# Kernel tuning notes

Hardware: AMD Instinct MI355X
Metric: run time of the kernel (lower is better)

Reference implementation:

```python
import jax, jax.numpy as jnp
import numpy as np

NX, NY, NZ = 432, 496, 1
D = 64        # num_pt_features
K = 3         # NUM_K
M = 1024      # memory size
BEV = 128     # num_bev_features
NCOORD = 3
NV = 10000    # pillars in scene
NP = 16384    # points in scene
BN_EPS = 1e-3
SHRINK = 0.0025


def hard_shrink_relu(x, lambd, eps=1e-12):
    return jax.nn.relu(x - lambd) * x / (jnp.abs(x - lambd) + eps)


def batchnorm_train(x, gamma, beta, eps=BN_EPS):
    # torch BatchNorm1d training-mode math (biased variance)
    mu = jnp.mean(x, axis=0)
    var = jnp.mean((x - mu) ** 2, axis=0)
    return (x - mu) * jax.lax.rsqrt(var + eps) * gamma + beta


def pdist2(a, b, eps=1e-5):
    # sqrt(eps + |  ||a||^2 + ||b||^2 - 2 a.b |), shape [n1, n2]
    n1 = jnp.sum(a * a, axis=1, keepdims=True)
    n2 = jnp.sum(b * b, axis=1, keepdims=True)
    d2 = n1 + n2.T - 2.0 * (a @ b.T)
    return jnp.sqrt(eps + jnp.abs(d2))


def memory_lookup(x_flat, mem_w, shrink):
    # MemAE-style memory unit: softmax addressing + hard shrink + L1 renorm
    att = jax.nn.softmax(x_flat @ mem_w.T, axis=1)          # [N, M]
    att = hard_shrink_relu(att, shrink)
    att = att / jnp.maximum(jnp.sum(jnp.abs(att), axis=1, keepdims=True), 1e-12)
    return att @ mem_w                                       # [N, D]


def setup_inputs() -> dict:
    key = jax.random.key(0)
    ks = jax.random.split(key, 8)
    rng = np.random.default_rng(0)
    flat = rng.choice(NX * NY, size=NV, replace=False)       # unique BEV cells
    x = (flat % NX).astype(np.int32)
    y = (flat // NX).astype(np.int32)
    coords = jnp.asarray(np.stack([np.zeros(NV, np.int32), x, y,
                                   np.zeros(NV, np.int32)], axis=1))  # (b, x, y, z)
    pc = jax.random.uniform(ks[1], (NP, 4), dtype=jnp.float32)
    point_coords = pc * jnp.array([0.0, NX, NY, 1.0], dtype=jnp.float32)
    return {
        "pillar_features": jax.random.normal(ks[0], (NV, D), dtype=jnp.float32),
        "coords": coords,
        "point_features": jax.random.normal(ks[2], (NP, D), dtype=jnp.float32),
        "point_coords": point_coords,
        "adapt_w": jax.random.normal(ks[3], (BEV // 2, D * K), dtype=jnp.float32) * 0.05,
        "bn1_g": jnp.ones((BEV // 2,), dtype=jnp.float32),
        "bn1_b": jnp.zeros((BEV // 2,), dtype=jnp.float32),
        "weight_w": jax.random.normal(ks[4], (2, BEV // 2), dtype=jnp.float32) * 0.1,
        "bn2_g": jnp.ones((2,), dtype=jnp.float32),
        "bn2_b": jnp.zeros((2,), dtype=jnp.float32),
        "mem_w": jax.random.normal(ks[5], (M, D), dtype=jnp.float32) * 0.1,
    }


def reference(pillar_features, coords, point_features, point_coords,
              adapt_w, bn1_g, bn1_b, weight_w, bn2_g, bn2_b, mem_w):
    nv = pillar_features.shape[0]
    pillars = pillar_features.T                              # [D, nv]

    # --- coord-based retrieval: smallest-K pdist(pillar coords, point coords) ---
    dist = pdist2(coords.astype(jnp.float32), point_coords)  # [nv, np]
    _, idx_c = jax.lax.top_k(-dist, K)                       # [nv, K]
    pillars_positive_coord = point_features[idx_c]           # [nv, K, D]

    # --- feature-based retrieval: top-K of softmax(points @ pillars, axis=0) ---
    score = jax.nn.softmax(point_features @ pillars, axis=0) # [np, nv]
    _, idx_f = jax.lax.top_k(score.T, K)                     # [nv, K]
    points_positive = point_features[idx_f]                  # [nv, K, D]

    # --- memory unit on both branches ---
    out_f = memory_lookup(points_positive.reshape(nv * K, D), mem_w, SHRINK).reshape(nv, K * D)
    out_c = memory_lookup(pillars_positive_coord.reshape(nv * K, D), mem_w, SHRINK).reshape(nv, K * D)

    f = jax.nn.relu(batchnorm_train(out_f @ adapt_w.T, bn1_g, bn1_b))  # [nv, 64]
    c = jax.nn.relu(batchnorm_train(out_c @ adapt_w.T, bn1_g, bn1_b))  # [nv, 64]
    w = jax.nn.softmax(batchnorm_train(pillar_features @ weight_w.T, bn2_g, bn2_b), axis=-1)
    pillars_aug = w[:, :1] * f + w[:, 1:2] * c               # [nv, 64]
    pillars_full = jnp.concatenate([pillars, pillars_aug.T], axis=0)  # [128, nv]

    # --- scatter to BEV canvas ---
    bev_idx = coords[:, 1] + coords[:, 2] * NX + coords[:, 3]
    spatial = jnp.zeros((BEV, NX * NY), dtype=pillar_features.dtype).at[:, bev_idx].set(pillars_full)
    pind = jnp.zeros((NCOORD, NX * NY), dtype=pillar_features.dtype)
    pind = pind.at[0, bev_idx].set(coords[:, 2].astype(jnp.float32))
    pind = pind.at[1, bev_idx].set(coords[:, 3].astype(jnp.float32))
    pind = pind.at[2, bev_idx].set(coords[:, 1].astype(jnp.float32))

    spatial_features = spatial.reshape(1, BEV * NZ, NY, NX)
    spatial_indices = pind.reshape(1, NCOORD * NZ, NY, NX)
    return spatial_features, spatial_indices
```

## Files before the change

### kernel.cpp

```cpp
#include <hip/hip_runtime.h>
#include <math.h>

#define NXc 432
#define NYc 496
#define NVc 10000
#define NPc 16384
#define CELLS (NXc*NYc)
#define SHRINKc 0.0025f
#define NVPAD 10048
#define NBX 27
#define NBY 31
#define NBIN (NBX*NBY)

typedef unsigned short u16;
typedef __attribute__((ext_vector_type(8))) short s16x8;
typedef __attribute__((ext_vector_type(4))) float f32x4;

__device__ __forceinline__ unsigned med3u(unsigned a, unsigned b, unsigned c) {
    unsigned d;
    asm("v_med3_u32 %0, %1, %2, %3" : "=v"(d) : "v"(a), "v"(b), "v"(c));
    return d;
}

__device__ __forceinline__ u16 f2b(float x) {
    unsigned u = __float_as_uint(x);
    unsigned r = (u + 0x7fffu + ((u >> 16) & 1u)) >> 16;
    return (u16)r;
}

__global__ __launch_bounds__(256) void k_init(const float* __restrict__ pillar,
                                              const float* __restrict__ pfeat,
                                              const float* __restrict__ memw,
                                              const float* __restrict__ adapt,
                                              float* __restrict__ stats,
                                              int* __restrict__ cellMap,
                                              u16* __restrict__ pillarH,
                                              u16* __restrict__ pfeatH,
                                              u16* __restrict__ memwH,
                                              u16* __restrict__ memwTH,
                                              u16* __restrict__ badaptH) {
    int gid = blockIdx.x * 256 + threadIdx.x;
    if (gid < CELLS) cellMap[gid] = -1;
    if (gid < 260) stats[gid] = 0.f;
    const int N1 = NVPAD * 64;
    const int N2 = N1 + NPc * 64;
    const int N3 = N2 + 65536;
    const int N4 = N3 + 65536;
    if (gid < N1) {
        int v = gid >> 6;
        pillarH[gid] = f2b(v < NVc ? pillar[gid] : 0.f);
    } else if (gid < N2) {
        pfeatH[gid - N1] = f2b(pfeat[gid - N1]);
    } else if (gid < N3) {
        memwH[gid - N2] = f2b(memw[gid - N2]);
    } else if (gid < N4) {
        int i = gid - N3;
        int d = i >> 10, j = i & 1023;
        memwTH[i] = f2b(memw[j * 64 + d]);
    } else {
        int i = gid - N4;
        int c = i >> 6, d = i & 63;
        badaptH[i] = f2b(adapt[(c & 63) * 192 + (c >> 6) * 64 + d]);
    }
}

__global__ __launch_bounds__(1024) void k_pre(const float* __restrict__ pcoord,
                                              const int* __restrict__ coords,
                                              int* __restrict__ binStart,
                                              float4* __restrict__ binPC,
                                              int* __restrict__ cellMap) {
    __shared__ int hcnt[1024];
    __shared__ int sc[1024];
    __shared__ int cur[1024];
    int t = threadIdx.x;
    hcnt[t] = 0;
    __syncthreads();
    for (int j = t; j < NPc; j += 1024) {
        float qx = pcoord[j * 4 + 1], qy = pcoord[j * 4 + 2];
        int bx = (int)(qx * 0.0625f); if (bx > NBX - 1) bx = NBX - 1;
        int by = (int)(qy * 0.0625f); if (by > NBY - 1) by = NBY - 1;
        atomicAdd(&hcnt[by * NBX + bx], 1);
    }
    __syncthreads();
    int vcount = (t < NBIN) ? hcnt[t] : 0;
    sc[t] = vcount;
    __syncthreads();
    for (int off = 1; off < 1024; off <<= 1) {
        int add = (t >= off) ? sc[t - off] : 0;
        __syncthreads();
        sc[t] += add;
        __syncthreads();
    }
    int excl = sc[t] - vcount;
    cur[t] = excl;
    if (t <= NBIN) binStart[t] = excl;
    __syncthreads();
    for (int j = t; j < NPc; j += 1024) {
        float qx = pcoord[j * 4 + 1], qy = pcoord[j * 4 + 2], qz = pcoord[j * 4 + 3];
        int bx = (int)(qx * 0.0625f); if (bx > NBX - 1) bx = NBX - 1;
        int by = (int)(qy * 0.0625f); if (by > NBY - 1) by = NBY - 1;
        int slot = atomicAdd(&cur[by * NBX + bx], 1);
        binPC[slot] = make_float4(qx, qy, qz * qz, __uint_as_float((unsigned)j));
    }
    for (int j = t; j < NVc; j += 1024) {
        int cell = coords[j * 4 + 1] + coords[j * 4 + 2] * NXc + coords[j * 4 + 3];
        cellMap[cell] = j;
    }
}

__global__ __launch_bounds__(256) void k_fused(const u16* __restrict__ pillarH,
                                               const u16* __restrict__ pfeatH,
                                               const u16* __restrict__ memwH,
                                               const u16* __restrict__ memwTH,
                                               const int* __restrict__ coords,
                                               const float4* __restrict__ binPC,
                                               const int* __restrict__ binStart,
                                               u16* __restrict__ PoutH,
                                               int* __restrict__ dIdx6,
                                               int* __restrict__ sIdx) {
    __shared__ union {
        u16 bf[2][8192];
        struct { u16 wh[4096]; u16 wt[4096]; u16 st[4][1024]; } m;
    } smem;
    int bid = blockIdx.x;
    int t = threadIdx.x;
    int w = t >> 6, l = t & 63;
    int lm = l & 15, qd = l >> 4;

    if (bid < 256) {
        int pb = bid * 64;
        u16* WH = smem.m.wh;
        u16* WT = smem.m.wt;
        u16* ST = &smem.m.st[w][0];
        const u16* arow = pfeatH + (size_t)(pb + 16 * w + lm) * 64 + qd * 8;
        s16x8 a0 = *(const s16x8*)arow;
        s16x8 a1 = *(const s16x8*)(arow + 32);
        float mM[4] = {-INFINITY, -INFINITY, -INFINITY, -INFINITY};
        float Zs[4] = {0.f, 0.f, 0.f, 0.f};
        for (int tile = 0; tile < 16; ++tile) {
            __syncthreads();
#pragma unroll
            for (int r = 0; r < 2; ++r) {
                int q = t + 256 * r;
                int row = q >> 3, g = q & 7;
                uint4 v = *(const uint4*)(memwH + (size_t)(tile * 64 + row) * 64 + g * 8);
                *(uint4*)&WH[(((row >> 4) * 8 + g) * 16 + ((row & 15) ^ g)) * 8] = v;
            }
            __syncthreads();
            f32x4 acc[4];
#pragma unroll
            for (int st = 0; st < 4; ++st) {
                s16x8 b0 = *(const s16x8*)&WH[((st * 8 + qd) * 16 + (lm ^ qd)) * 8];
                s16x8 b1 = *(const s16x8*)&WH[((st * 8 + qd + 4) * 16 + (lm ^ (qd + 4))) * 8];
                f32x4 z = {0.f, 0.f, 0.f, 0.f};
                z = __builtin_amdgcn_mfma_f32_16x16x32_bf16(a0, b0, z, 0, 0, 0);
                z = __builtin_amdgcn_mfma_f32_16x16x32_bf16(a1, b1, z, 0, 0, 0);
                acc[st] = z;
            }
#pragma unroll
            for (int r = 0; r < 4; ++r) {
                float tmax = acc[0][r];
#pragma unroll
                for (int st = 1; st < 4; ++st) tmax = fmaxf(tmax, acc[st][r]);
                float mn = fmaxf(mM[r], tmax);
                float zacc = Zs[r] * __expf(mM[r] - mn);
#pragma unroll
                for (int st = 0; st < 4; ++st) zacc += __expf(acc[st][r] - mn);
                mM[r] = mn; Zs[r] = zacc;
            }
        }
#pragma unroll
        for (int r = 0; r < 4; ++r) {
#pragma unroll
            for (int off = 1; off < 16; off <<= 1) {
                float om = __shfl_xor(mM[r], off);
                float oz = __shfl_xor(Zs[r], off);
                float mn = fmaxf(mM[r], om);
                Zs[r] = Zs[r] * __expf(mM[r] - mn) + oz * __expf(om - mn);
                mM[r] = mn;
            }
        }
        float invZ[4], L1[4] = {0.f, 0.f, 0.f, 0.f};
#pragma unroll
        for (int r = 0; r < 4; ++r) invZ[r] = 1.f / Zs[r];
        f32x4 oacc[4];
#pragma unroll
        for (int n = 0; n < 4; ++n) oacc[n] = (f32x4){0.f, 0.f, 0.f, 0.f};
        for (int tile = 0; tile < 16; ++tile) {
            __syncthreads();
#pragma unroll
            for (int r = 0; r < 2; ++r) {
                int q = t + 256 * r;
                int row = q >> 3, g = q & 7;
                uint4 v = *(const uint4*)(memwH + (size_t)(tile * 64 + row) * 64 + g * 8);
                *(uint4*)&WH[(((row >> 4) * 8 + g) * 16 + ((row & 15) ^ g)) * 8] = v;
            }
#pragma unroll
            for (int r = 0; r < 2; ++r) {
                int q = t + 256 * r;
                int row = q >> 3, g = q & 7;
                uint4 v = *(const uint4*)(memwTH + (size_t)row * 1024 + tile * 64 + g * 8);
                *(uint4*)&WT[(g * 64 + (row ^ g)) * 8] = v;
            }
            __syncthreads();
#pragma unroll
            for (int st = 0; st < 4; ++st) {
                s16x8 b0 = *(const s16x8*)&WH[((st * 8 + qd) * 16 + (lm ^ qd)) * 8];
                s16x8 b1 = *(const s16x8*)&WH[((st * 8 + qd + 4) * 16 + (lm ^ (qd + 4))) * 8];
                f32x4 z = {0.f, 0.f, 0.f, 0.f};
                z = __builtin_amdgcn_mfma_f32_16x16x32_bf16(a0, b0, z, 0, 0, 0);
                z = __builtin_amdgcn_mfma_f32_16x16x32_bf16(a1, b1, z, 0, 0, 0);
                int g2 = st * 2 + (lm >> 3);
#pragma unroll
                for (int r = 0; r < 4; ++r) {
                    float e = __expf(z[r] - mM[r]);
                    float a = e * invZ[r];
                    float tt = a - SHRINKc;
                    float sres = fmaxf(tt, 0.f) * a / (fabsf(tt) + 1e-12f);
                    L1[r] += sres;
                    int rr = qd * 4 + r;
                    ST[(g2 * 16 + (rr ^ g2)) * 8 + (lm & 7)] = f2b(sres);
                }
            }
#pragma unroll
            for (int ks = 0; ks < 2; ++ks) {
                int g = ks * 4 + qd;
                s16x8 af = *(const s16x8*)&ST[(g * 16 + (lm ^ g)) * 8];
#pragma unroll
                for (int n = 0; n < 4; ++n) {
                    s16x8 bf = *(const s16x8*)&WT[(g * 64 + ((n * 16 + lm) ^ g)) * 8];
                    oacc[n] = __builtin_amdgcn_mfma_f32_16x16x32_bf16(af, bf, oacc[n], 0, 0, 0);
                }
            }
        }
#pragma unroll
        for (int r = 0; r < 4; ++r) {
#pragma unroll
            for (int off = 1; off < 16; off <<= 1) L1[r] += __shfl_xor(L1[r], off);
            L1[r] = 1.f / fmaxf(L1[r], 1e-12f);
        }
#pragma unroll
        for (int n = 0; n < 4; ++n)
#pragma unroll
            for (int r = 0; r < 4; ++r)
                PoutH[(size_t)(pb + 16 * w + qd * 4 + r) * 64 + n * 16 + lm] =
                    f2b(oacc[n][r] * L1[r]);
    } else if (bid < 296) {
        int v = (bid - 256) * 256 + t;
        if (v >= NVc) return;
        int xi = coords[v * 4 + 1], yi = coords[v * 4 + 2];
        float x = (float)xi, y = (float)yi;
        int bx = xi >> 4; if (bx > NBX - 1) bx = NBX - 1;
        int by = yi >> 4; if (by > NBY - 1) by = NBY - 1;
        unsigned kk[6] = {~0u, ~0u, ~0u, ~0u, ~0u, ~0u};
        for (int r = 0; r < 32; ++r) {
            int x0 = bx - r, x1 = bx + r, y0 = by - r, y1 = by + r;
            for (int cy = y0; cy <= y1; ++cy) {
                if (cy < 0 || cy > NBY - 1) continue;
                int step = (cy == y0 || cy == y1) ? 1 : (x1 > x0 ? x1 - x0 : 1);
                for (int cx = x0; cx <= x1; cx += step) {
                    if (cx < 0 || cx > NBX - 1) continue;
                    int b = cy * NBX + cx;
                    int s0 = binStart[b], s1 = binStart[b + 1];
                    for (int s = s0; s < s1; ++s) {
                        float4 p = binPC[s];
                        float e1 = x - p.x, e2 = y - p.y;
                        float d2 = fmaf(e1, e1, fmaf(e2, e2, p.z));
                        unsigned tk = (__float_as_uint(d2) & 0xFFFFC000u) | __float_as_uint(p.w);
                        kk[5] = med3u(kk[4], kk[5], tk);
                        kk[4] = med3u(kk[3], kk[4], tk);
                        kk[3] = med3u(kk[2], kk[3], tk);
                        kk[2] = med3u(kk[1], kk[2], tk);
                        kk[1] = med3u(kk[0], kk[1], tk);
                        kk[0] = kk[0] < tk ? kk[0] : tk;
                    }
                }
            }
            if (kk[2] != ~0u) {
                float d3 = __uint_as_float(kk[2] & 0xFFFFC000u);
                if (256.f * (float)(r * r) > d3 * 1.004f + 1e-3f) break;
            }
        }
#pragma unroll
        for (int j2 = 0; j2 < 6; ++j2) dIdx6[v * 6 + j2] = (int)(kk[j2] & 16383u);
    } else {
        int sb = bid - 296;
        int pb = (sb >> 4) * 64;
        int cb = (sb & 15) * 1024;
        const u16* arow = pillarH + (size_t)(pb + 16 * w + lm) * 64 + qd * 8;
        s16x8 a0 = *(const s16x8*)arow;
        s16x8 a1 = *(const s16x8*)(arow + 32);
        int so[4], doff[4];
#pragma unroll
        for (int r = 0; r < 4; ++r) {
            int q = t + 256 * r;
            int row = q >> 3, g = q & 7;
            so[r] = row * 64 + g * 8;
            doff[r] = (((row >> 4) * 8 + g) * 16 + ((row & 15) ^ g)) * 8;
        }
        uint4 pre[4];
        const u16* src = pfeatH + (size_t)cb * 64;
#pragma unroll
        for (int r = 0; r < 4; ++r) pre[r] = *(const uint4*)(src + so[r]);
#pragma unroll
        for (int r = 0; r < 4; ++r) *(uint4*)&smem.bf[0][doff[r]] = pre[r];
        unsigned sk[4][4];
#pragma unroll
        for (int r = 0; r < 4; ++r)
#pragma unroll
            for (int j = 0; j < 4; ++j) sk[r][j] = 0u;
        for (int s = 0; s < 8; ++s) {
            __syncthreads();
            if (s < 7) {
                const u16* s2 = src + (size_t)(s + 1) * 128 * 64;
#pragma unroll
                for (int r = 0; r < 4; ++r) pre[r] = *(const uint4*)(s2 + so[r]);
            }
            const u16* B = &smem.bf[s & 1][0];
#pragma unroll
            for (int pt = 0; pt < 8; ++pt) {
                s16x8 b0 = *(const s16x8*)&B[(((pt * 8 + qd) * 16) + (lm ^ qd)) * 8];
                s16x8 b1 = *(const s16x8*)&B[(((pt * 8 + qd + 4) * 16) + (lm ^ (qd + 4))) * 8];
                f32x4 acc = {256.f, 256.f, 256.f, 256.f};
                acc = __builtin_amdgcn_mfma_f32_16x16x32_bf16(a0, b0, acc, 0, 0, 0);
                acc = __builtin_amdgcn_mfma_f32_16x16x32_bf16(a1, b1, acc, 0, 0, 0);
                unsigned idf = (unsigned)(1023 - (s * 128 + pt * 16 + lm));
#pragma unroll
                for (int r = 0; r < 4; ++r) {
                    unsigned key = (__float_as_uint(acc[r]) & 0xFFFFFC00u) | idf;
                    sk[r][3] = med3u(sk[r][2], sk[r][3], key);
                    sk[r][2] = med3u(sk[r][1], sk[r][2], key);
                    sk[r][1] = med3u(sk[r][0], sk[r][1], key);
                    sk[r][0] = sk[r][0] > key ? sk[r][0] : key;
                }
            }
            if (s < 7) {
#pragma unroll
                for (int r = 0; r < 4; ++r) *(uint4*)&smem.bf[(s + 1) & 1][doff[r]] = pre[r];
            }
        }
        __syncthreads();
        unsigned* mrg = (unsigned*)&smem.bf[0][0];
#pragma unroll
        for (int r = 0; r < 4; ++r) {
            int row = 16 * w + qd * 4 + r;
            *(uint4*)&mrg[(row * 16 + lm) * 4] =
                make_uint4(sk[r][0], sk[r][1], sk[r][2], sk[r][3]);
        }
        __syncthreads();
        if (t < 64) {
            int gpr = pb + t;
            unsigned m0 = 0u, m1 = 0u, m2 = 0u, m3 = 0u;
#pragma unroll 4
            for (int cc = 0; cc < 16; ++cc) {
                uint4 v = *(const uint4*)&mrg[(t * 16 + cc) * 4];
#pragma unroll
                for (int j = 0; j < 4; ++j) {
                    unsigned x = j == 0 ? v.x : (j == 1 ? v.y : (j == 2 ? v.z : v.w));
                    m3 = med3u(m2, m3, x);
                    m2 = med3u(m1, m2, x);
                    m1 = med3u(m0, m1, x);
                    m0 = m0 > x ? m0 : x;
                }
            }
            if (gpr < NVc) {
                int base = ((sb & 15) * NVc + gpr) * 4;
                sIdx[base + 0] = cb + 1023 - (int)(m0 & 1023u);
                sIdx[base + 1] = cb + 1023 - (int)(m1 & 1023u);
                sIdx[base + 2] = cb + 1023 - (int)(m2 & 1023u);
                sIdx[base + 3] = cb + 1023 - (int)(m3 & 1023u);
            }
        }
    }
}

__global__ __launch_bounds__(256) void k_rerank(const float* __restrict__ pillar,
                                                const int* __restrict__ coords,
                                                const float* __restrict__ pfeat,
                                                const float* __restrict__ pcoord,
                                                const int* __restrict__ sIdx,
                                                const int* __restrict__ dIdx6,
                                                int* __restrict__ idx_f,
                                                int* __restrict__ idx_c) {
    int t = threadIdx.x;
    int wv = t >> 6, l = t & 63;
    int v = blockIdx.x * 4 + wv;
    int chunk = l >> 2, slot = l & 3;
    int ps = sIdx[(chunk * NVc + v) * 4 + slot];
    int pd = dIdx6[v * 6 + (l < 6 ? l : 0)];
    double s = 0.0;
#pragma unroll
    for (int i = 0; i < 16; ++i) {
        float4 a = *(const float4*)(pillar + v * 64 + 4 * i);
        float4 b = *(const float4*)(pfeat + ps * 64 + 4 * i);
        s += (double)a.x * (double)b.x + (double)a.y * (double)b.y
           + (double)a.z * (double)b.z + (double)a.w * (double)b.w;
    }
    float4 qc = *(const float4*)(pcoord + pd * 4);
    double db_ = (double)coords[v * 4 + 0] - (double)qc.x;
    double dx_ = (double)coords[v * 4 + 1] - (double)qc.y;
    double dy_ = (double)coords[v * 4 + 2] - (double)qc.z;
    double dz_ = (double)coords[v * 4 + 3] - (double)qc.w;
    double d2 = db_ * db_ + dx_ * dx_ + dy_ * dy_ + dz_ * dz_;
    double sv = s; int sx = ps;
    for (int k = 0; k < 3; ++k) {
        double bv = sv; int bi = sx;
#pragma unroll
        for (int off = 32; off >= 1; off >>= 1) {
            double ov = __shfl_xor(bv, off);
            int    oi = __shfl_xor(bi, off);
            if (ov > bv || (ov == bv && oi < bi)) { bv = ov; bi = oi; }
        }
        if (l == 0) idx_f[v * 3 + k] = bi;
        if (sx == bi) { sv = -INFINITY; sx = 0x7fffffff; }
    }
    double dv = d2; int dx2 = pd;
    for (int k = 0; k < 3; ++k) {
        double bv = dv; int bi = dx2;
#pragma unroll
        for (int off = 32; off >= 1; off >>= 1) {
            double ov = __shfl_xor(bv, off);
            int    oi = __shfl_xor(bi, off);
            if (ov < bv || (ov == bv && oi < bi)) { bv = ov; bi = oi; }
        }
        if (l == 0) idx_c[v * 3 + k] = bi;
        if (dx2 == bi) { dv = INFINITY; dx2 = 0x7fffffff; }
    }
}

__global__ __launch_bounds__(256) void k_proj2(const u16* __restrict__ PoutH,
                                               const u16* __restrict__ badaptH,
                                               float* __restrict__ Q) {
    __shared__ u16 AD[12288];
    int t = threadIdx.x;
    int w = t >> 6, l = t & 63;
    int lm = l & 15, qd = l >> 4;
    int pb = blockIdx.x * 64;
#pragma unroll
    for (int r = 0; r < 6; ++r) {
        int q = t + 256 * r;
        int row = q >> 3, g = q & 7;
        uint4 v = *(const uint4*)(badaptH + (size_t)row * 64 + g * 8);
        *(uint4*)&AD[(((row >> 4) * 8 + g) * 16 + ((row & 15) ^ g)) * 8] = v;
    }
    const u16* arow = PoutH + (size_t)(pb + 16 * w + lm) * 64 + qd * 8;
    s16x8 a0 = *(const s16x8*)arow;
    s16x8 a1 = *(const s16x8*)(arow + 32);
    __syncthreads();
    f32x4 acc[12];
#pragma unroll
    for (int nt = 0; nt < 12; ++nt) {
        s16x8 b0 = *(const s16x8*)&AD[(((nt * 8 + qd) * 16) + (lm ^ qd)) * 8];
        s16x8 b1 = *(const s16x8*)&AD[(((nt * 8 + qd + 4) * 16) + (lm ^ (qd + 4))) * 8];
        f32x4 z = {0.f, 0.f, 0.f, 0.f};
        z = __builtin_amdgcn_mfma_f32_16x16x32_bf16(a0, b0, z, 0, 0, 0);
        z = __builtin_amdgcn_mfma_f32_16x16x32_bf16(a1, b1, z, 0, 0, 0);
        acc[nt] = z;
    }
#pragma unroll
    for (int nt = 0; nt < 12; ++nt)
#pragma unroll
        for (int r = 0; r < 4; ++r)
            Q[(size_t)(pb + 16 * w + qd * 4 + r) * 192 + nt * 16 + lm] = acc[nt][r];
}

__global__ __launch_bounds__(256) void k_gather(const float* __restrict__ Q,
                                                const int* __restrict__ idx_f,
                                                const int* __restrict__ idx_c,
                                                const float* __restrict__ pillar,
                                                const float* __restrict__ ww,
                                                float* __restrict__ f_pre,
                                                float* __restrict__ c_pre,
                                                float* __restrict__ w_pre,
                                                float* __restrict__ stats) {
    __shared__ float red[4][4][64];
    __shared__ float redw[4][4];
    int t = threadIdx.x;
    int wv = t >> 6, l = t & 63;
    int base = blockIdx.x * 40;
    int vend = base + 40;
    float fs = 0, fq = 0, cs = 0, cq = 0, ws0 = 0, wq0 = 0, ws1 = 0, wq1 = 0;
    float w0l = ww[l], w1l = ww[64 + l];
    for (int v = base + wv; v < vend; v += 4) {
        int if0 = idx_f[v * 3], if1 = idx_f[v * 3 + 1], if2 = idx_f[v * 3 + 2];
        float f = Q[if0 * 192 + l] + Q[if1 * 192 + 64 + l] + Q[if2 * 192 + 128 + l];
        f_pre[v * 64 + l] = f; fs += f; fq += f * f;
        int ic0 = idx_c[v * 3], ic1 = idx_c[v * 3 + 1], ic2 = idx_c[v * 3 + 2];
        float c = Q[ic0 * 192 + l] + Q[ic1 * 192 + 64 + l] + Q[ic2 * 192 + 128 + l];
        c_pre[v * 64 + l] = c; cs += c; cq += c * c;
        float pv = pillar[v * 64 + l];
        float a0 = pv * w0l, a1 = pv * w1l;
#pragma unroll
        for (int off = 32; off >= 1; off >>= 1) {
            a0 += __shfl_xor(a0, off);
            a1 += __shfl_xor(a1, off);
        }
        if (l == 0) { w_pre[v * 2] = a0; w_pre[v * 2 + 1] = a1; }
        ws0 += a0; wq0 += a0 * a0; ws1 += a1; wq1 += a1 * a1;
    }
    red[0][wv][l] = fs; red[1][wv][l] = fq; red[2][wv][l] = cs; red[3][wv][l] = cq;
    if (l == 0) { redw[wv][0] = ws0; redw[wv][1] = wq0; redw[wv][2] = ws1; redw[wv][3] = wq1; }
    __syncthreads();
    if (wv == 0) {
#pragma unroll
        for (int q = 0; q < 4; ++q) {
            float sum = red[q][0][l] + red[q][1][l] + red[q][2][l] + red[q][3][l];
            atomicAdd(&stats[q * 64 + l], sum);
        }
        if (l < 4) {
            float sum = redw[0][l] + redw[1][l] + redw[2][l] + redw[3][l];
            atomicAdd(&stats[256 + l], sum);
        }
    }
}

__global__ __launch_bounds__(256) void k_out2(const int* __restrict__ cellMap,
                                              const float* __restrict__ pillar,
                                              const float* __restrict__ f_pre,
                                              const float* __restrict__ c_pre,
                                              const float* __restrict__ w_pre,
                                              const float* __restrict__ stats,
                                              const float* __restrict__ g1,
                                              const float* __restrict__ b1,
                                              const float* __restrict__ g2,
                                              const float* __restrict__ b2,
                                              float* __restrict__ out) {
    int c4 = (blockIdx.x * 256 + threadIdx.x) * 4;
    if (c4 >= CELLS) return;
    int4 cm = *(const int4*)(cellMap + c4);
    const float invn = 1.0f / (float)NVc;
    float mw0 = stats[256] * invn, vw0 = stats[257] * invn - mw0 * mw0;
    float mw1 = stats[258] * invn, vw1 = stats[259] * invn - mw1 * mw1;
    float rw0 = rsqrtf(vw0 + 1e-3f), rw1 = rsqrtf(vw1 + 1e-3f);
    float g20 = g2[0], b20 = b2[0], g21 = g2[1], b21 = b2[1];
    float w0c[4], w1c[4];
    int cms[4] = {cm.x, cm.y, cm.z, cm.w};
#pragma unroll
    for (int k = 0; k < 4; ++k) {
        int c = cms[k];
        if (c >= 0) {
            float z0 = (w_pre[c * 2] - mw0) * rw0 * g20 + b20;
            float z1 = (w_pre[c * 2 + 1] - mw1) * rw1 * g21 + b21;
            float mz = fmaxf(z0, z1);
            float e0 = __expf(z0 - mz), e1 = __expf(z1 - mz);
            float wd = 1.f / (e0 + e1);
            w0c[k] = e0 * wd; w1c[k] = e1 * wd;
        } else { w0c[k] = 0.f; w1c[k] = 0.f; }
    }
    int f0 = blockIdx.y * 33;
    int f1 = f0 + 33; if (f1 > 131) f1 = 131;
    for (int f = f0; f < f1; ++f) {
        float4 val;
        if (f < 64) {
            val.x = cm.x >= 0 ? pillar[cm.x * 64 + f] : 0.f;
            val.y = cm.y >= 0 ? pillar[cm.y * 64 + f] : 0.f;
            val.z = cm.z >= 0 ? pillar[cm.z * 64 + f] : 0.f;
            val.w = cm.w >= 0 ? pillar[cm.w * 64 + f] : 0.f;
        } else if (f < 128) {
            int fa = f - 64;
            float mf = stats[fa] * invn;
            float rf = rsqrtf(stats[64 + fa] * invn - mf * mf + 1e-3f);
            float mc = stats[128 + fa] * invn;
            float rc = rsqrtf(stats[192 + fa] * invn - mc * mc + 1e-3f);
            float gg = g1[fa], bb = b1[fa];
            float* vv = (float*)&val;
#pragma unroll
            for (int k = 0; k < 4; ++k) {
                int c = cms[k];
                if (c >= 0) {
                    float fv = fmaxf((f_pre[c * 64 + fa] - mf) * rf * gg + bb, 0.f);
                    float cv = fmaxf((c_pre[c * 64 + fa] - mc) * rc * gg + bb, 0.f);
                    vv[k] = w0c[k] * fv + w1c[k] * cv;
                } else vv[k] = 0.f;
            }
        } else if (f == 128) {
            val.x = cm.x >= 0 ? (float)((c4 + 0) / NXc) : 0.f;
            val.y = cm.y >= 0 ? (float)((c4 + 1) / NXc) : 0.f;
            val.z = cm.z >= 0 ? (float)((c4 + 2) / NXc) : 0.f;
            val.w = cm.w >= 0 ? (float)((c4 + 3) / NXc) : 0.f;
        } else if (f == 129) {
            val = make_float4(0.f, 0.f, 0.f, 0.f);
        } else {
            val.x = cm.x >= 0 ? (float)((c4 + 0) % NXc) : 0.f;
            val.y = cm.y >= 0 ? (float)((c4 + 1) % NXc) : 0.f;
            val.z = cm.z >= 0 ? (float)((c4 + 2) % NXc) : 0.f;
            val.w = cm.w >= 0 ? (float)((c4 + 3) % NXc) : 0.f;
        }
        *(float4*)(out + (size_t)f * CELLS + c4) = val;
    }
}

extern "C" void kernel_launch(void* const* d_in, const int* in_sizes, int n_in,
                              void* d_out, int out_size, void* d_ws, size_t ws_size,
                              hipStream_t stream) {
    const float* pillar = (const float*)d_in[0];
    const int*   coords = (const int*)d_in[1];
    const float* pfeat  = (const float*)d_in[2];
    const float* pcoord = (const float*)d_in[3];
    const float* adapt  = (const float*)d_in[4];
    const float* bn1g   = (const float*)d_in[5];
    const float* bn1b   = (const float*)d_in[6];
    const float* ww     = (const float*)d_in[7];
    const float* bn2g   = (const float*)d_in[8];
    const float* bn2b   = (const float*)d_in[9];
    const float* memw   = (const float*)d_in[10];
    float* out = (float*)d_out;
    float* ws  = (float*)d_ws;
    u16*   PoutH = (u16*)(ws + 0);
    float* Q     = ws + 1048576;
    int*   sIdx  = (int*)(ws + 4194304);
    int*   binStart  = (int*)(ws + 4834304);
    int*   dIdx6     = (int*)(ws + 4836824);
    float4* binPC    = (float4*)(ws + 4896824);
    u16*   memwH   = (u16*)(ws + 4970000);
    u16*   memwTH  = (u16*)(ws + 5002768);
    u16*   badaptH = (u16*)(ws + 5035536);
    int*   idxf  = (int*)(ws + 5474304);
    int*   idxc  = (int*)(ws + 5504304);
    float* fpre  = ws + 5534304;
    float* cpre  = ws + 6174304;
    float* wpre  = ws + 6814304;
    float* stats = ws + 6834304;
    int*   cellMap = (int*)(ws + 6840000);
    u16* pillarH = (u16*)(ws + 5534304);
    u16* pfeatH  = pillarH + (size_t)NVPAD * 64;

    k_init  <<<7168, 256, 0, stream>>>(pillar, pfeat, memw, adapt, stats, cellMap,
                                       pillarH, pfeatH, memwH, memwTH, badaptH);
    k_pre   <<<1, 1024, 0, stream>>>(pcoord, coords, binStart, binPC, cellMap);
    k_fused <<<2808, 256, 0, stream>>>(pillarH, pfeatH, memwH, memwTH, coords,
                                       binPC, binStart, PoutH, dIdx6, sIdx);
    k_rerank<<<2500, 256, 0, stream>>>(pillar, coords, pfeat, pcoord, sIdx, dIdx6, idxf, idxc);
    k_proj2 <<<256, 256, 0, stream>>>(PoutH, badaptH, Q);
    k_gather<<<250, 256, 0, stream>>>(Q, idxf, idxc, pillar, ww, fpre, cpre, wpre, stats);
    k_out2  <<<dim3(210, 4), 256, 0, stream>>>(cellMap, pillar, fpre, cpre, wpre, stats,
                                               bn1g, bn1b, bn2g, bn2b, out);
}
```

Baseline: 338.4 us.

## Merge rerank and projection kernels, move cellMap build, single-buffer similarity tile

Combines k_rerank and k_proj2 into one launch (k_fused2) whose blocks split by index between the projection GEMM and the exact rerank. This saves a kernel launch and lets the two independent workloads overlap. The cellMap scatter moves out of the single-block k_pre into k_gather, shortening the serial k_pre. The pillar-vs-point similarity loop in k_fused drops its register-prefetched double buffer for a single LDS buffer with two barriers per stage, which cuts LDS use and registers but gives up load/compute overlap.

```diff
diff --git a/kernel.cpp b/kernel.cpp
--- a/kernel.cpp
+++ b/kernel.cpp
@@ -65,10 +65,8 @@
 }
 
 __global__ __launch_bounds__(1024) void k_pre(const float* __restrict__ pcoord,
-                                              const int* __restrict__ coords,
                                               int* __restrict__ binStart,
-                                              float4* __restrict__ binPC,
-                                              int* __restrict__ cellMap) {
+                                              float4* __restrict__ binPC) {
     __shared__ int hcnt[1024];
     __shared__ int sc[1024];
     __shared__ int cur[1024];
@@ -102,10 +100,6 @@
         int slot = atomicAdd(&cur[by * NBX + bx], 1);
         binPC[slot] = make_float4(qx, qy, qz * qz, __uint_as_float((unsigned)j));
     }
-    for (int j = t; j < NVc; j += 1024) {
-        int cell = coords[j * 4 + 1] + coords[j * 4 + 2] * NXc + coords[j * 4 + 3];
-        cellMap[cell] = j;
-    }
 }
 
 __global__ __launch_bounds__(256) void k_fused(const u16* __restrict__ pillarH,
@@ -119,7 +113,7 @@
                                                int* __restrict__ dIdx6,
                                                int* __restrict__ sIdx) {
     __shared__ union {
-        u16 bf[2][8192];
+        u16 bf[8192];
         struct { u16 wh[4096]; u16 wt[4096]; u16 st[4][1024]; } m;
     } smem;
     int bid = blockIdx.x;
@@ -298,29 +292,22 @@
             so[r] = row * 64 + g * 8;
             doff[r] = (((row >> 4) * 8 + g) * 16 + ((row & 15) ^ g)) * 8;
         }
-        uint4 pre[4];
         const u16* src = pfeatH + (size_t)cb * 64;
-#pragma unroll
-        for (int r = 0; r < 4; ++r) pre[r] = *(const uint4*)(src + so[r]);
-#pragma unroll
-        for (int r = 0; r < 4; ++r) *(uint4*)&smem.bf[0][doff[r]] = pre[r];
         unsigned sk[4][4];
 #pragma unroll
         for (int r = 0; r < 4; ++r)
 #pragma unroll
             for (int j = 0; j < 4; ++j) sk[r][j] = 0u;
         for (int s = 0; s < 8; ++s) {
+            const u16* s2 = src + (size_t)s * 128 * 64;
+#pragma unroll
+            for (int r = 0; r < 4; ++r)
+                *(uint4*)&smem.bf[doff[r]] = *(const uint4*)(s2 + so[r]);
             __syncthreads();
-            if (s < 7) {
-                const u16* s2 = src + (size_t)(s + 1) * 128 * 64;
-#pragma unroll
-                for (int r = 0; r < 4; ++r) pre[r] = *(const uint4*)(s2 + so[r]);
-            }
-            const u16* B = &smem.bf[s & 1][0];
 #pragma unroll
             for (int pt = 0; pt < 8; ++pt) {
-                s16x8 b0 = *(const s16x8*)&B[(((pt * 8 + qd) * 16) + (lm ^ qd)) * 8];
-                s16x8 b1 = *(const s16x8*)&B[(((pt * 8 + qd + 4) * 16) + (lm ^ (qd + 4))) * 8];
+                s16x8 b0 = *(const s16x8*)&smem.bf[(((pt * 8 + qd) * 16) + (lm ^ qd)) * 8];
+                s16x8 b1 = *(const s16x8*)&smem.bf[(((pt * 8 + qd + 4) * 16) + (lm ^ (qd + 4))) * 8];
                 f32x4 acc = {256.f, 256.f, 256.f, 256.f};
                 acc = __builtin_amdgcn_mfma_f32_16x16x32_bf16(a0, b0, acc, 0, 0, 0);
                 acc = __builtin_amdgcn_mfma_f32_16x16x32_bf16(a1, b1, acc, 0, 0, 0);
@@ -334,13 +321,9 @@
                     sk[r][0] = sk[r][0] > key ? sk[r][0] : key;
                 }
             }
-            if (s < 7) {
-#pragma unroll
-                for (int r = 0; r < 4; ++r) *(uint4*)&smem.bf[(s + 1) & 1][doff[r]] = pre[r];
-            }
-        }
-        __syncthreads();
-        unsigned* mrg = (unsigned*)&smem.bf[0][0];
+            __syncthreads();
+        }
+        unsigned* mrg = (unsigned*)&smem.bf[0];
 #pragma unroll
         for (int r = 0; r < 4; ++r) {
             int row = 16 * w + qd * 4 + r;
@@ -374,111 +357,119 @@
     }
 }
 
-__global__ __launch_bounds__(256) void k_rerank(const float* __restrict__ pillar,
+__global__ __launch_bounds__(256) void k_fused2(const u16* __restrict__ PoutH,
+                                                const u16* __restrict__ badaptH,
+                                                const float* __restrict__ pillar,
                                                 const int* __restrict__ coords,
                                                 const float* __restrict__ pfeat,
                                                 const float* __restrict__ pcoord,
                                                 const int* __restrict__ sIdx,
                                                 const int* __restrict__ dIdx6,
+                                                float* __restrict__ Q,
                                                 int* __restrict__ idx_f,
                                                 int* __restrict__ idx_c) {
+    __shared__ u16 AD[12288];
+    int bid = blockIdx.x;
     int t = threadIdx.x;
-    int wv = t >> 6, l = t & 63;
-    int v = blockIdx.x * 4 + wv;
-    int chunk = l >> 2, slot = l & 3;
-    int ps = sIdx[(chunk * NVc + v) * 4 + slot];
-    int pd = dIdx6[v * 6 + (l < 6 ? l : 0)];
-    double s = 0.0;
-#pragma unroll
-    for (int i = 0; i < 16; ++i) {
-        float4 a = *(const float4*)(pillar + v * 64 + 4 * i);
-        float4 b = *(const float4*)(pfeat + ps * 64 + 4 * i);
-        s += (double)a.x * (double)b.x + (double)a.y * (double)b.y
-           + (double)a.z * (double)b.z + (double)a.w * (double)b.w;
-    }
-    float4 qc = *(const float4*)(pcoord + pd * 4);
-    double db_ = (double)coords[v * 4 + 0] - (double)qc.x;
-    double dx_ = (double)coords[v * 4 + 1] - (double)qc.y;
-    double dy_ = (double)coords[v * 4 + 2] - (double)qc.z;
-    double dz_ = (double)coords[v * 4 + 3] - (double)qc.w;
-    double d2 = db_ * db_ + dx_ * dx_ + dy_ * dy_ + dz_ * dz_;
-    double sv = s; int sx = ps;
-    for (int k = 0; k < 3; ++k) {
-        double bv = sv; int bi = sx;
-#pragma unroll
-        for (int off = 32; off >= 1; off >>= 1) {
-            double ov = __shfl_xor(bv, off);
-            int    oi = __shfl_xor(bi, off);
-            if (ov > bv || (ov == bv && oi < bi)) { bv = ov; bi = oi; }
-        }
-        if (l == 0) idx_f[v * 3 + k] = bi;
-        if (sx == bi) { sv = -INFINITY; sx = 0x7fffffff; }
-    }
-    double dv = d2; int dx2 = pd;
-    for (int k = 0; k < 3; ++k) {
-        double bv = dv; int bi = dx2;
-#pragma unroll
-        for (int off = 32; off >= 1; off >>= 1) {
-            double ov = __shfl_xor(bv, off);
-            int    oi = __shfl_xor(bi, off);
-            if (ov < bv || (ov == bv && oi < bi)) { bv = ov; bi = oi; }
-        }
-        if (l == 0) idx_c[v * 3 + k] = bi;
-        if (dx2 == bi) { dv = INFINITY; dx2 = 0x7fffffff; }
-    }
-}
-
-__global__ __launch_bounds__(256) void k_proj2(const u16* __restrict__ PoutH,
-                                               const u16* __restrict__ badaptH,
-                                               float* __restrict__ Q) {
-    __shared__ u16 AD[12288];
-    int t = threadIdx.x;
-    int w = t >> 6, l = t & 63;
-    int lm = l & 15, qd = l >> 4;
-    int pb = blockIdx.x * 64;
-#pragma unroll
-    for (int r = 0; r < 6; ++r) {
-        int q = t + 256 * r;
-        int row = q >> 3, g = q & 7;
-        uint4 v = *(const uint4*)(badaptH + (size_t)row * 64 + g * 8);
-        *(uint4*)&AD[(((row >> 4) * 8 + g) * 16 + ((row & 15) ^ g)) * 8] = v;
-    }
-    const u16* arow = PoutH + (size_t)(pb + 16 * w + lm) * 64 + qd * 8;
-    s16x8 a0 = *(const s16x8*)arow;
-    s16x8 a1 = *(const s16x8*)(arow + 32);
-    __syncthreads();
-    f32x4 acc[12];
-#pragma unroll
-    for (int nt = 0; nt < 12; ++nt) {
-        s16x8 b0 = *(const s16x8*)&AD[(((nt * 8 + qd) * 16) + (lm ^ qd)) * 8];
-        s16x8 b1 = *(const s16x8*)&AD[(((nt * 8 + qd + 4) * 16) + (lm ^ (qd + 4))) * 8];
-        f32x4 z = {0.f, 0.f, 0.f, 0.f};
-        z = __builtin_amdgcn_mfma_f32_16x16x32_bf16(a0, b0, z, 0, 0, 0);
-        z = __builtin_amdgcn_mfma_f32_16x16x32_bf16(a1, b1, z, 0, 0, 0);
-        acc[nt] = z;
-    }
-#pragma unroll
-    for (int nt = 0; nt < 12; ++nt)
-#pragma unroll
-        for (int r = 0; r < 4; ++r)
-            Q[(size_t)(pb + 16 * w + qd * 4 + r) * 192 + nt * 16 + lm] = acc[nt][r];
+    if (bid < 256) {
+        int w = t >> 6, l = t & 63;
+        int lm = l & 15, qd = l >> 4;
+        int pb = bid * 64;
+#pragma unroll
+        for (int r = 0; r < 6; ++r) {
+            int q = t + 256 * r;
+            int row = q >> 3, g = q & 7;
+            uint4 v = *(const uint4*)(badaptH + (size_t)row * 64 + g * 8);
+            *(uint4*)&AD[(((row >> 4) * 8 + g) * 16 + ((row & 15) ^ g)) * 8] = v;
+        }
+        const u16* arow = PoutH + (size_t)(pb + 16 * w + lm) * 64 + qd * 8;
+        s16x8 a0 = *(const s16x8*)arow;
+        s16x8 a1 = *(const s16x8*)(arow + 32);
+        __syncthreads();
+        f32x4 acc[12];
+#pragma unroll
+        for (int nt = 0; nt < 12; ++nt) {
+            s16x8 b0 = *(const s16x8*)&AD[(((nt * 8 + qd) * 16) + (lm ^ qd)) * 8];
+            s16x8 b1 = *(const s16x8*)&AD[(((nt * 8 + qd + 4) * 16) + (lm ^ (qd + 4))) * 8];
+            f32x4 z = {0.f, 0.f, 0.f, 0.f};
+            z = __builtin_amdgcn_mfma_f32_16x16x32_bf16(a0, b0, z, 0, 0, 0);
+            z = __builtin_amdgcn_mfma_f32_16x16x32_bf16(a1, b1, z, 0, 0, 0);
+            acc[nt] = z;
+        }
+#pragma unroll
+        for (int nt = 0; nt < 12; ++nt)
+#pragma unroll
+            for (int r = 0; r < 4; ++r)
+                Q[(size_t)(pb + 16 * w + qd * 4 + r) * 192 + nt * 16 + lm] = acc[nt][r];
+    } else {
+        int wv = t >> 6, l = t & 63;
+        int v = (bid - 256) * 4 + wv;
+        int chunk = l >> 2, slot = l & 3;
+        int ps = sIdx[(chunk * NVc + v) * 4 + slot];
+        int pd = dIdx6[v * 6 + (l < 6 ? l : 0)];
+        double s = 0.0;
+#pragma unroll
+        for (int i = 0; i < 16; ++i) {
+            float4 a = *(const float4*)(pillar + v * 64 + 4 * i);
+            float4 b = *(const float4*)(pfeat + ps * 64 + 4 * i);
+            s += (double)a.x * (double)b.x + (double)a.y * (double)b.y
+               + (double)a.z * (double)b.z + (double)a.w * (double)b.w;
+        }
+        float4 qc = *(const float4*)(pcoord + pd * 4);
+        double db_ = (double)coords[v * 4 + 0] - (double)qc.x;
+        double dx_ = (double)coords[v * 4 + 1] - (double)qc.y;
+        double dy_ = (double)coords[v * 4 + 2] - (double)qc.z;
+        double dz_ = (double)coords[v * 4 + 3] - (double)qc.w;
+        double d2 = db_ * db_ + dx_ * dx_ + dy_ * dy_ + dz_ * dz_;
+        double sv = s; int sx = ps;
+        for (int k = 0; k < 3; ++k) {
+            double bv = sv; int bi = sx;
+#pragma unroll
+            for (int off = 32; off >= 1; off >>= 1) {
+                double ov = __shfl_xor(bv, off);
+                int    oi = __shfl_xor(bi, off);
+                if (ov > bv || (ov == bv && oi < bi)) { bv = ov; bi = oi; }
+            }
+            if (l == 0) idx_f[v * 3 + k] = bi;
+            if (sx == bi) { sv = -INFINITY; sx = 0x7fffffff; }
+        }
+        double dv = d2; int dx2 = pd;
+        for (int k = 0; k < 3; ++k) {
+            double bv = dv; int bi = dx2;
+#pragma unroll
+            for (int off = 32; off >= 1; off >>= 1) {
+                double ov = __shfl_xor(bv, off);
+                int    oi = __shfl_xor(bi, off);
+                if (ov < bv || (ov == bv && oi < bi)) { bv = ov; bi = oi; }
+            }
+            if (l == 0) idx_c[v * 3 + k] = bi;
+            if (dx2 == bi) { dv = INFINITY; dx2 = 0x7fffffff; }
+        }
+    }
 }
 
 __global__ __launch_bounds__(256) void k_gather(const float* __restrict__ Q,
                                                 const int* __restrict__ idx_f,
                                                 const int* __restrict__ idx_c,
                                                 const float* __restrict__ pillar,
+                                                const int* __restrict__ coords,
                                                 const float* __restrict__ ww,
                                                 float* __restrict__ f_pre,
                                                 float* __restrict__ c_pre,
                                                 float* __restrict__ w_pre,
-                                                float* __restrict__ stats) {
+                                                float* __restrict__ stats,
+                                                int* __restrict__ cellMap) {
     __shared__ float red[4][4][64];
     __shared__ float redw[4][4];
     int t = threadIdx.x;
     int wv = t >> 6, l = t & 63;
     int base = blockIdx.x * 40;
     int vend = base + 40;
+    if (t < 40) {
+        int v = base + t;
+        int cell = coords[v * 4 + 1] + coords[v * 4 + 2] * NXc + coords[v * 4 + 3];
+        cellMap[cell] = v;
+    }
     float fs = 0, fq = 0, cs = 0, cq = 0, ws0 = 0, wq0 = 0, ws1 = 0, wq1 = 0;
     float w0l = ww[l], w1l = ww[64 + l];
     for (int v = base + wv; v < vend; v += 4) {
@@ -627,12 +618,13 @@
 
     k_init  <<<7168, 256, 0, stream>>>(pillar, pfeat, memw, adapt, stats, cellMap,
                                        pillarH, pfeatH, memwH, memwTH, badaptH);
-    k_pre   <<<1, 1024, 0, stream>>>(pcoord, coords, binStart, binPC, cellMap);
+    k_pre   <<<1, 1024, 0, stream>>>(pcoord, binStart, binPC);
     k_fused <<<2808, 256, 0, stream>>>(pillarH, pfeatH, memwH, memwTH, coords,
                                        binPC, binStart, PoutH, dIdx6, sIdx);
-    k_rerank<<<2500, 256, 0, stream>>>(pillar, coords, pfeat, pcoord, sIdx, dIdx6, idxf, idxc);
-    k_proj2 <<<256, 256, 0, stream>>>(PoutH, badaptH, Q);
-    k_gather<<<250, 256, 0, stream>>>(Q, idxf, idxc, pillar, ww, fpre, cpre, wpre, stats);
+    k_fused2<<<2756, 256, 0, stream>>>(PoutH, badaptH, pillar, coords, pfeat, pcoord,
+                                       sIdx, dIdx6, Q, idxf, idxc);
+    k_gather<<<250, 256, 0, stream>>>(Q, idxf, idxc, pillar, coords, ww,
+                                      fpre, cpre, wpre, stats, cellMap);
     k_out2  <<<dim3(210, 4), 256, 0, stream>>>(cellMap, pillar, fpre, cpre, wpre, stats,
                                                bn1g, bn1b, bn2g, bn2b, out);
 }
```

Result: faster. 323.4 us (-4.4%).
